# Kernel optimization log

Hardware: AMD Instinct MI355X
Metric: run time of the kernel (lower is better)

## Reference

```python
import jax, jax.numpy as jnp
import numpy as np
from jax import lax

M, T, WINDOW = 4096, 2048, 25
NEG_DIAG = -1e10  # matches alphas.fill_diagonal_(-1e10)


def setup_inputs() -> dict:
    key = jax.random.key(0)
    k_ys, k_a, k_r, k_b0, k_b1 = jax.random.split(key, 5)
    ys = jax.random.uniform(k_ys, (M, T), dtype=jnp.float32) * 10.0  # case counts
    alphas = 0.01 * jax.random.normal(k_a, (M, M), dtype=jnp.float32)
    repro = 1.0 + 0.01 * jax.random.normal(k_r, (M, WINDOW), dtype=jnp.float32)  # init ones
    b0 = 0.1 * jax.random.normal(k_b0, (M, 1), dtype=jnp.float32)
    b1 = 0.01 * jax.random.normal(k_b1, (M, 1), dtype=jnp.float32)
    t = jnp.arange(T, dtype=jnp.int32) + 1
    return {"ys": ys, "alphas": alphas, "repro": repro, "b0": b0, "b1": b1, "t": t}


def reference(ys, alphas, repro, b0, b1, t):
    m, _ = ys.shape
    window = repro.shape[1]
    offset = window - 1
    # metapopulation weights: sigmoid adjacency with diagonal forced to ~0
    diag = jnp.eye(m, dtype=bool)
    W = jax.nn.sigmoid(jnp.where(diag, jnp.asarray(NEG_DIAG, ys.dtype), alphas))
    # depthwise conv1d (cross-correlation), groups=M, VALID padding -> (M, T-window+1)
    Z = lax.conv_general_dilated(
        ys[None],                 # (1, M, T)
        repro[:, None, :],        # (M, 1, window)
        window_strides=(1,),
        padding='VALID',
        feature_group_count=m,
        dimension_numbers=('NCH', 'OIH', 'NCH'),
    )[0]                          # (M, T')
    ys_n = ys[:, offset:]         # (M, T')
    # beta_net: per-node softplus-linear in time -> (M, T), then narrow
    tt = t.astype(ys.dtype)
    beta = jax.nn.softplus(b0 + b1 * tt[None, :])[:, offset:]  # (M, T')
    return beta * (jax.nn.softplus(Z) + W @ ys_n)
```

## Files before the change

kernel.cpp:

```cpp
#include <hip/hip_runtime.h>
#include <stdint.h>

#define M_DIM 4096
#define T_DIM 2048
#define N_OUT 2024
#define N_PAD 2048
#define WIN   25
#define K_DIM 4096

typedef float f32x4 __attribute__((ext_vector_type(4)));

__device__ __forceinline__ unsigned short f2bf(float x) {
  unsigned u = __float_as_uint(x);
  u += 0x7FFF + ((u >> 16) & 1);
  return (unsigned short)(u >> 16);
}
__device__ __forceinline__ float bf2f(unsigned short h) {
  return __uint_as_float(((unsigned)h) << 16);
}

__device__ __forceinline__ void gl2lds16(const void* g, void* l) {
  __builtin_amdgcn_global_load_lds(
      (const __attribute__((address_space(1))) unsigned int*)g,
      (__attribute__((address_space(3))) unsigned int*)l, 16, 0, 0);
}

__device__ __forceinline__ int pk_fp8x4(float a, float b, float c, float d) {
  int w = __builtin_amdgcn_cvt_pk_fp8_f32(a, b, 0, false);
  w = __builtin_amdgcn_cvt_pk_fp8_f32(c, d, w, true);
  return w;
}

__global__ __launch_bounds__(256) void k_wcast(const float* __restrict__ alphas,
                                               unsigned char* __restrict__ W8) {
  size_t i8 = ((size_t)blockIdx.x * 256 + threadIdx.x) * 8;
  const float4 v0 = *(const float4*)(alphas + i8);
  const float4 v1 = *(const float4*)(alphas + i8 + 4);
  int row = (int)(i8 >> 12);
  int col = (int)(i8 & 4095);
  float a[8] = {v0.x, v0.y, v0.z, v0.w, v1.x, v1.y, v1.z, v1.w};
  float w[8];
#pragma unroll
  for (int j = 0; j < 8; ++j)
    w[j] = (row == col + j) ? 0.f : 1.f / (1.f + __expf(-a[j]));
  int p0 = pk_fp8x4(w[0], w[1], w[2], w[3]);
  int p1 = pk_fp8x4(w[4], w[5], w[6], w[7]);
  *(uint2*)(W8 + i8) = uint2{(unsigned)p0, (unsigned)p1};
}

__global__ __launch_bounds__(256) void k_conv(const float* __restrict__ ys,
                                              const float* __restrict__ repro,
                                              unsigned short* __restrict__ Sbf) {
  __shared__ float sy[256 + WIN - 1];
  __shared__ float sr[WIN];
  int m = blockIdx.y;
  int j0 = blockIdx.x * 256;
  int tid = threadIdx.x;
  sy[tid] = ys[(size_t)m * T_DIM + j0 + tid];
  if (tid < WIN - 1) {
    int jj = j0 + 256 + tid;
    sy[256 + tid] = (jj < T_DIM) ? ys[(size_t)m * T_DIM + jj] : 0.f;
  }
  if (tid < WIN) sr[tid] = repro[m * WIN + tid];
  __syncthreads();
  int j = j0 + tid;
  float z = 0.f;
#pragma unroll
  for (int k = 0; k < WIN; ++k) z += sy[tid + k] * sr[k];
  float sp = fmaxf(z, 0.f) + log1pf(__expf(-fabsf(z)));
  Sbf[(size_t)m * N_PAD + j] = (j < N_OUT) ? f2bf(sp) : (unsigned short)0;
}

__global__ __launch_bounds__(256) void k_transpose(const float* __restrict__ ys,
                                                   unsigned char* __restrict__ BT8) {
  __shared__ float t[64][65];
  int n0 = blockIdx.x * 64;
  int k0 = blockIdx.y * 64;
  int tx = threadIdx.x;
  int ty = threadIdx.y;
#pragma unroll
  for (int r = 0; r < 16; ++r) {
    int kk = k0 + ty + r * 4;
    int n = n0 + tx;
    t[ty + r * 4][tx] = (n < N_OUT) ? ys[(size_t)kk * T_DIM + n + (WIN - 1)] : 0.f;
  }
  __syncthreads();
  int tid = ty * 64 + tx;
  int nl = tid >> 2;
  int kc = (tid & 3) * 16;
  unsigned wds[4];
#pragma unroll
  for (int w = 0; w < 4; ++w)
    wds[w] = (unsigned)pk_fp8x4(t[kc + 4 * w][nl], t[kc + 4 * w + 1][nl],
                                t[kc + 4 * w + 2][nl], t[kc + 4 * w + 3][nl]);
  *(uint4*)(BT8 + (size_t)(n0 + nl) * K_DIM + k0 + kc) =
      uint4{wds[0], wds[1], wds[2], wds[3]};
}

__global__ __launch_bounds__(512, 4) void k_gemm(const unsigned char* __restrict__ W8,
                                                 const unsigned char* __restrict__ BT8,
                                                 const unsigned short* __restrict__ Sbf,
                                                 const float* __restrict__ b0,
                                                 const float* __restrict__ b1,
                                                 float* __restrict__ out) {
  __shared__ __align__(64) unsigned char lA[4][128 * 64];
  __shared__ __align__(64) unsigned char lB[4][128 * 64];
  const int tid  = threadIdx.x;
  const int wave = tid >> 6;
  const int lane = tid & 63;
  const int wm = wave >> 2;
  const int wn = wave & 3;
  const int m16  = lane & 15;
  const int quad = lane >> 4;

  const int fid  = blockIdx.y * gridDim.x + blockIdx.x;
  const int swz  = (fid & 7) * 64 + (fid >> 3);
  const int tileN = (swz & 15) * 128;
  const int tileM = (swz >> 4) * 128;

  const int key  = (m16 >> 1) & 3;
  const int sub  = (quad & 1) * 8;
  const int rowA = (wm * 64 + m16) * 64;
  const int rowB = (wn * 32 + m16) * 64;
  int hOf[2];
#pragma unroll
  for (int h = 0; h < 2; ++h)
    hOf[h] = (((2 * h + (quad >> 1)) ^ key) << 4) + sub;

  const int o = wave * 1024 + lane * 16;
  const int r = o >> 6;
  const int s = (o >> 4) & 3;
  const int q = s ^ ((r >> 1) & 3);
  const unsigned char* gA = W8  + (size_t)(tileM + r) * K_DIM + q * 16;
  const unsigned char* gB = BT8 + (size_t)(tileN + r) * K_DIM + q * 16;
  const int ldsOff = wave * 1024;

  f32x4 acc[4][2];
#pragma unroll
  for (int i = 0; i < 4; ++i)
#pragma unroll
    for (int j = 0; j < 2; ++j) acc[i][j] = f32x4{0.f, 0.f, 0.f, 0.f};

  auto stage = [&](int buf, int kt_) {
    const size_t kb_ = (size_t)kt_ * 64;
    gl2lds16(gA + kb_, &lA[buf][ldsOff]);
    gl2lds16(gB + kb_, &lB[buf][ldsOff]);
  };
  auto compute = [&](int buf) {
#pragma unroll
    for (int h = 0; h < 2; ++h) {
      long long aF[4], bF[2];
#pragma unroll
      for (int i = 0; i < 4; ++i)
        aF[i] = *(const long long*)&lA[buf][rowA + i * 1024 + hOf[h]];
#pragma unroll
      for (int j = 0; j < 2; ++j)
        bF[j] = *(const long long*)&lB[buf][rowB + j * 1024 + hOf[h]];
#pragma unroll
      for (int i = 0; i < 4; ++i)
#pragma unroll
        for (int j = 0; j < 2; ++j)
          acc[i][j] = __builtin_amdgcn_mfma_f32_16x16x32_fp8_fp8(
              aF[i], bF[j], acc[i][j], 0, 0, 0);
    }
  };

  stage(0, 0);
  stage(1, 1);
  stage(2, 2);

#pragma unroll 1
  for (int kt = 0; kt < K_DIM / 64; kt += 4) {
    stage(3, kt + 3);
    asm volatile("s_waitcnt vmcnt(6)" ::: "memory");
    __builtin_amdgcn_s_barrier();
    asm volatile("" ::: "memory");
    compute(0);
    __builtin_amdgcn_s_barrier();
    asm volatile("" ::: "memory");

    if (kt + 4 < K_DIM / 64) {
      stage(0, kt + 4);
      asm volatile("s_waitcnt vmcnt(6)" ::: "memory");
    } else {
      asm volatile("s_waitcnt vmcnt(4)" ::: "memory");
    }
    __builtin_amdgcn_s_barrier();
    asm volatile("" ::: "memory");
    compute(1);
    __builtin_amdgcn_s_barrier();
    asm volatile("" ::: "memory");

    if (kt + 5 < K_DIM / 64) {
      stage(1, kt + 5);
      asm volatile("s_waitcnt vmcnt(6)" ::: "memory");
    } else {
      asm volatile("s_waitcnt vmcnt(2)" ::: "memory");
    }
    __builtin_amdgcn_s_barrier();
    asm volatile("" ::: "memory");
    compute(2);
    __builtin_amdgcn_s_barrier();
    asm volatile("" ::: "memory");

    if (kt + 6 < K_DIM / 64) {
      stage(2, kt + 6);
      asm volatile("s_waitcnt vmcnt(6)" ::: "memory");
    } else {
      asm volatile("s_waitcnt vmcnt(0)" ::: "memory");
    }
    __builtin_amdgcn_s_barrier();
    asm volatile("" ::: "memory");
    compute(3);
    __builtin_amdgcn_s_barrier();
    asm volatile("" ::: "memory");
  }

#pragma unroll
  for (int j = 0; j < 2; ++j) {
    int gn = tileN + wn * 32 + j * 16 + m16;
    if (gn >= N_OUT) continue;
    float tval = (float)(gn + WIN);
#pragma unroll
    for (int i = 0; i < 4; ++i) {
#pragma unroll
      for (int r2 = 0; r2 < 4; ++r2) {
        int gm = tileM + wm * 64 + i * 16 + quad * 4 + r2;
        float x = b0[gm] + b1[gm] * tval;
        float beta = fmaxf(x, 0.f) + log1pf(__expf(-fabsf(x)));
        float sv = bf2f(Sbf[(size_t)gm * N_PAD + gn]);
        out[(size_t)gm * N_OUT + gn] = beta * (sv + acc[i][j][r2]);
      }
    }
  }
}

extern "C" void kernel_launch(void* const* d_in, const int* in_sizes, int n_in,
                              void* d_out, int out_size, void* d_ws, size_t ws_size,
                              hipStream_t stream) {
  const float* ys     = (const float*)d_in[0];
  const float* alphas = (const float*)d_in[1];
  const float* repro  = (const float*)d_in[2];
  const float* b0     = (const float*)d_in[3];
  const float* b1     = (const float*)d_in[4];
  float* out = (float*)d_out;

  char* ws = (char*)d_ws;
  unsigned char*  W8  = (unsigned char*)ws;
  unsigned char*  BT8 = (unsigned char*)(ws + (size_t)M_DIM * K_DIM);
  unsigned short* Sbf = (unsigned short*)(ws + (size_t)M_DIM * K_DIM
                                             + (size_t)N_PAD * K_DIM);

  k_wcast<<<(M_DIM * (size_t)K_DIM) / 8 / 256, 256, 0, stream>>>(alphas, W8);
  k_conv<<<dim3(T_DIM / 256, M_DIM), 256, 0, stream>>>(ys, repro, Sbf);
  k_transpose<<<dim3(N_PAD / 64, K_DIM / 64), dim3(64, 4), 0, stream>>>(ys, BT8);
  k_gemm<<<dim3(N_PAD / 128, M_DIM / 128), 512, 0, stream>>>(W8, BT8, Sbf, b0, b1, out);
}
```

Baseline: 252.7 us.

## Split-K GEMM with atomic accumulation and fuse prep kernels into one launch

Merges the weight cast, convolution, transpose and a new output-zeroing pass into a single block-dispatched prep kernel, which removes launch overhead. The GEMM now splits K into two halves across a third grid dimension, doubling the block count, and accumulates into the output with atomic adds. The LDS pipeline shrinks from four stages to two so more blocks fit per CU (launch bounds raised to 8). The cost is an extra zeroing pass over the output, atomic traffic on every output element, and a shallower prefetch pipeline.

```diff
diff --git a/kernel.cpp b/kernel.cpp
--- a/kernel.cpp
+++ b/kernel.cpp
@@ -7,6 +7,7 @@
 #define N_PAD 2048
 #define WIN   25
 #define K_DIM 4096
+#define K_HALF 2048
 
 typedef float f32x4 __attribute__((ext_vector_type(4)));
 
@@ -31,80 +32,96 @@
   return w;
 }
 
-__global__ __launch_bounds__(256) void k_wcast(const float* __restrict__ alphas,
-                                               unsigned char* __restrict__ W8) {
-  size_t i8 = ((size_t)blockIdx.x * 256 + threadIdx.x) * 8;
-  const float4 v0 = *(const float4*)(alphas + i8);
-  const float4 v1 = *(const float4*)(alphas + i8 + 4);
-  int row = (int)(i8 >> 12);
-  int col = (int)(i8 & 4095);
-  float a[8] = {v0.x, v0.y, v0.z, v0.w, v1.x, v1.y, v1.z, v1.w};
-  float w[8];
-#pragma unroll
-  for (int j = 0; j < 8; ++j)
-    w[j] = (row == col + j) ? 0.f : 1.f / (1.f + __expf(-a[j]));
-  int p0 = pk_fp8x4(w[0], w[1], w[2], w[3]);
-  int p1 = pk_fp8x4(w[4], w[5], w[6], w[7]);
-  *(uint2*)(W8 + i8) = uint2{(unsigned)p0, (unsigned)p1};
-}
-
-__global__ __launch_bounds__(256) void k_conv(const float* __restrict__ ys,
+#define NB_WCAST 8192
+#define NB_CONV  32768
+#define NB_TRANS 2048
+#define NB_ZERO  8096
+#define B_CONV   NB_WCAST
+#define B_TRANS  (B_CONV + NB_CONV)
+#define B_ZERO   (B_TRANS + NB_TRANS)
+#define NB_PREP  (B_ZERO + NB_ZERO)
+
+__global__ __launch_bounds__(256) void k_prep(const float* __restrict__ alphas,
+                                              const float* __restrict__ ys,
                                               const float* __restrict__ repro,
-                                              unsigned short* __restrict__ Sbf) {
-  __shared__ float sy[256 + WIN - 1];
-  __shared__ float sr[WIN];
-  int m = blockIdx.y;
-  int j0 = blockIdx.x * 256;
-  int tid = threadIdx.x;
-  sy[tid] = ys[(size_t)m * T_DIM + j0 + tid];
-  if (tid < WIN - 1) {
-    int jj = j0 + 256 + tid;
-    sy[256 + tid] = (jj < T_DIM) ? ys[(size_t)m * T_DIM + jj] : 0.f;
+                                              unsigned char* __restrict__ W8,
+                                              unsigned char* __restrict__ BT8,
+                                              unsigned short* __restrict__ Sbf,
+                                              float* __restrict__ out) {
+  __shared__ __align__(16) char smem[64 * 65 * 4];
+  const int bid = blockIdx.x;
+  const int tid = threadIdx.x;
+
+  if (bid < B_CONV) {
+    size_t i8 = ((size_t)bid * 256 + tid) * 8;
+    const float4 v0 = *(const float4*)(alphas + i8);
+    const float4 v1 = *(const float4*)(alphas + i8 + 4);
+    int row = (int)(i8 >> 12);
+    int col = (int)(i8 & 4095);
+    float a[8] = {v0.x, v0.y, v0.z, v0.w, v1.x, v1.y, v1.z, v1.w};
+    float w[8];
+#pragma unroll
+    for (int j = 0; j < 8; ++j)
+      w[j] = (row == col + j) ? 0.f : 1.f / (1.f + __expf(-a[j]));
+    int p0 = pk_fp8x4(w[0], w[1], w[2], w[3]);
+    int p1 = pk_fp8x4(w[4], w[5], w[6], w[7]);
+    *(uint2*)(W8 + i8) = uint2{(unsigned)p0, (unsigned)p1};
+  } else if (bid < B_TRANS) {
+    float* sy = (float*)smem;
+    float* sr = sy + 280;
+    int b  = bid - B_CONV;
+    int m  = b >> 3;
+    int j0 = (b & 7) * 256;
+    sy[tid] = ys[(size_t)m * T_DIM + j0 + tid];
+    if (tid < WIN - 1) {
+      int jj = j0 + 256 + tid;
+      sy[256 + tid] = (jj < T_DIM) ? ys[(size_t)m * T_DIM + jj] : 0.f;
+    }
+    if (tid < WIN) sr[tid] = repro[m * WIN + tid];
+    __syncthreads();
+    int j = j0 + tid;
+    float z = 0.f;
+#pragma unroll
+    for (int k = 0; k < WIN; ++k) z += sy[tid + k] * sr[k];
+    float sp = fmaxf(z, 0.f) + log1pf(__expf(-fabsf(z)));
+    Sbf[(size_t)m * N_PAD + j] = (j < N_OUT) ? f2bf(sp) : (unsigned short)0;
+  } else if (bid < B_ZERO) {
+    float (*t)[65] = (float (*)[65])smem;
+    int b  = bid - B_TRANS;
+    int n0 = (b & 31) * 64;
+    int k0 = (b >> 5) * 64;
+    int tx = tid & 63;
+    int ty = tid >> 6;
+#pragma unroll
+    for (int r = 0; r < 16; ++r) {
+      int kk = k0 + ty + r * 4;
+      int n = n0 + tx;
+      t[ty + r * 4][tx] = (n < N_OUT) ? ys[(size_t)kk * T_DIM + n + (WIN - 1)] : 0.f;
+    }
+    __syncthreads();
+    int nl = tid >> 2;
+    int kc = (tid & 3) * 16;
+    unsigned wds[4];
+#pragma unroll
+    for (int w = 0; w < 4; ++w)
+      wds[w] = (unsigned)pk_fp8x4(t[kc + 4 * w][nl], t[kc + 4 * w + 1][nl],
+                                  t[kc + 4 * w + 2][nl], t[kc + 4 * w + 3][nl]);
+    *(uint4*)(BT8 + (size_t)(n0 + nl) * K_DIM + k0 + kc) =
+        uint4{wds[0], wds[1], wds[2], wds[3]};
+  } else {
+    size_t idx = ((size_t)(bid - B_ZERO) * 256 + tid);
+    ((float4*)out)[idx] = float4{0.f, 0.f, 0.f, 0.f};
   }
-  if (tid < WIN) sr[tid] = repro[m * WIN + tid];
-  __syncthreads();
-  int j = j0 + tid;
-  float z = 0.f;
-#pragma unroll
-  for (int k = 0; k < WIN; ++k) z += sy[tid + k] * sr[k];
-  float sp = fmaxf(z, 0.f) + log1pf(__expf(-fabsf(z)));
-  Sbf[(size_t)m * N_PAD + j] = (j < N_OUT) ? f2bf(sp) : (unsigned short)0;
-}
-
-__global__ __launch_bounds__(256) void k_transpose(const float* __restrict__ ys,
-                                                   unsigned char* __restrict__ BT8) {
-  __shared__ float t[64][65];
-  int n0 = blockIdx.x * 64;
-  int k0 = blockIdx.y * 64;
-  int tx = threadIdx.x;
-  int ty = threadIdx.y;
-#pragma unroll
-  for (int r = 0; r < 16; ++r) {
-    int kk = k0 + ty + r * 4;
-    int n = n0 + tx;
-    t[ty + r * 4][tx] = (n < N_OUT) ? ys[(size_t)kk * T_DIM + n + (WIN - 1)] : 0.f;
-  }
-  __syncthreads();
-  int tid = ty * 64 + tx;
-  int nl = tid >> 2;
-  int kc = (tid & 3) * 16;
-  unsigned wds[4];
-#pragma unroll
-  for (int w = 0; w < 4; ++w)
-    wds[w] = (unsigned)pk_fp8x4(t[kc + 4 * w][nl], t[kc + 4 * w + 1][nl],
-                                t[kc + 4 * w + 2][nl], t[kc + 4 * w + 3][nl]);
-  *(uint4*)(BT8 + (size_t)(n0 + nl) * K_DIM + k0 + kc) =
-      uint4{wds[0], wds[1], wds[2], wds[3]};
-}
-
-__global__ __launch_bounds__(512, 4) void k_gemm(const unsigned char* __restrict__ W8,
+}
+
+__global__ __launch_bounds__(512, 8) void k_gemm(const unsigned char* __restrict__ W8,
                                                  const unsigned char* __restrict__ BT8,
                                                  const unsigned short* __restrict__ Sbf,
                                                  const float* __restrict__ b0,
                                                  const float* __restrict__ b1,
                                                  float* __restrict__ out) {
-  __shared__ __align__(64) unsigned char lA[4][128 * 64];
-  __shared__ __align__(64) unsigned char lB[4][128 * 64];
+  __shared__ __align__(64) unsigned char lA[2][128 * 64];
+  __shared__ __align__(64) unsigned char lB[2][128 * 64];
   const int tid  = threadIdx.x;
   const int wave = tid >> 6;
   const int lane = tid & 63;
@@ -113,10 +130,11 @@
   const int m16  = lane & 15;
   const int quad = lane >> 4;
 
-  const int fid  = blockIdx.y * gridDim.x + blockIdx.x;
-  const int swz  = (fid & 7) * 64 + (fid >> 3);
+  const int fid = (blockIdx.z * 32 + blockIdx.y) * 16 + blockIdx.x;
+  const int swz = (fid & 7) * 128 + (fid >> 3);
+  const int kh    = swz >> 9;
+  const int tileM = ((swz >> 4) & 31) * 128;
   const int tileN = (swz & 15) * 128;
-  const int tileM = (swz >> 4) * 128;
 
   const int key  = (m16 >> 1) & 3;
   const int sub  = (quad & 1) * 8;
@@ -131,8 +149,8 @@
   const int r = o >> 6;
   const int s = (o >> 4) & 3;
   const int q = s ^ ((r >> 1) & 3);
-  const unsigned char* gA = W8  + (size_t)(tileM + r) * K_DIM + q * 16;
-  const unsigned char* gB = BT8 + (size_t)(tileN + r) * K_DIM + q * 16;
+  const unsigned char* gA = W8  + (size_t)(tileM + r) * K_DIM + kh * K_HALF + q * 16;
+  const unsigned char* gB = BT8 + (size_t)(tileN + r) * K_DIM + kh * K_HALF + q * 16;
   const int ldsOff = wave * 1024;
 
   f32x4 acc[4][2];
@@ -166,52 +184,26 @@
   };
 
   stage(0, 0);
-  stage(1, 1);
-  stage(2, 2);
 
 #pragma unroll 1
-  for (int kt = 0; kt < K_DIM / 64; kt += 4) {
-    stage(3, kt + 3);
-    asm volatile("s_waitcnt vmcnt(6)" ::: "memory");
+  for (int kt = 0; kt < K_HALF / 64; kt += 2) {
+    stage(1, kt + 1);
+    asm volatile("s_waitcnt vmcnt(2)" ::: "memory");
     __builtin_amdgcn_s_barrier();
     asm volatile("" ::: "memory");
     compute(0);
     __builtin_amdgcn_s_barrier();
     asm volatile("" ::: "memory");
 
-    if (kt + 4 < K_DIM / 64) {
-      stage(0, kt + 4);
-      asm volatile("s_waitcnt vmcnt(6)" ::: "memory");
-    } else {
-      asm volatile("s_waitcnt vmcnt(4)" ::: "memory");
-    }
-    __builtin_amdgcn_s_barrier();
-    asm volatile("" ::: "memory");
-    compute(1);
-    __builtin_amdgcn_s_barrier();
-    asm volatile("" ::: "memory");
-
-    if (kt + 5 < K_DIM / 64) {
-      stage(1, kt + 5);
-      asm volatile("s_waitcnt vmcnt(6)" ::: "memory");
-    } else {
+    if (kt + 2 < K_HALF / 64) {
+      stage(0, kt + 2);
       asm volatile("s_waitcnt vmcnt(2)" ::: "memory");
-    }
-    __builtin_amdgcn_s_barrier();
-    asm volatile("" ::: "memory");
-    compute(2);
-    __builtin_amdgcn_s_barrier();
-    asm volatile("" ::: "memory");
-
-    if (kt + 6 < K_DIM / 64) {
-      stage(2, kt + 6);
-      asm volatile("s_waitcnt vmcnt(6)" ::: "memory");
     } else {
       asm volatile("s_waitcnt vmcnt(0)" ::: "memory");
     }
     __builtin_amdgcn_s_barrier();
     asm volatile("" ::: "memory");
-    compute(3);
+    compute(1);
     __builtin_amdgcn_s_barrier();
     asm volatile("" ::: "memory");
   }
@@ -228,8 +220,9 @@
         int gm = tileM + wm * 64 + i * 16 + quad * 4 + r2;
         float x = b0[gm] + b1[gm] * tval;
         float beta = fmaxf(x, 0.f) + log1pf(__expf(-fabsf(x)));
-        float sv = bf2f(Sbf[(size_t)gm * N_PAD + gn]);
-        out[(size_t)gm * N_OUT + gn] = beta * (sv + acc[i][j][r2]);
+        float sv = (kh == 0) ? bf2f(Sbf[(size_t)gm * N_PAD + gn]) : 0.f;
+        unsafeAtomicAdd(&out[(size_t)gm * N_OUT + gn],
+                        beta * (sv + acc[i][j][r2]));
       }
     }
   }
@@ -251,8 +244,7 @@
   unsigned short* Sbf = (unsigned short*)(ws + (size_t)M_DIM * K_DIM
                                              + (size_t)N_PAD * K_DIM);
 
-  k_wcast<<<(M_DIM * (size_t)K_DIM) / 8 / 256, 256, 0, stream>>>(alphas, W8);
-  k_conv<<<dim3(T_DIM / 256, M_DIM), 256, 0, stream>>>(ys, repro, Sbf);
-  k_transpose<<<dim3(N_PAD / 64, K_DIM / 64), dim3(64, 4), 0, stream>>>(ys, BT8);
-  k_gemm<<<dim3(N_PAD / 128, M_DIM / 128), 512, 0, stream>>>(W8, BT8, Sbf, b0, b1, out);
-}
+  k_prep<<<NB_PREP, 256, 0, stream>>>(alphas, ys, repro, W8, BT8, Sbf, out);
+  k_gemm<<<dim3(N_PAD / 128, M_DIM / 128, 2), 512, 0, stream>>>(W8, BT8, Sbf,
+                                                                b0, b1, out);
+}
```

Result: slower. 368.8 us (+46.0%).

## Merge prep kernels into one launch and widen GEMM block to 16 waves

Applied to the files above, without the earlier changes.

The W cast, conv/softplus and transpose kernels are folded into one launch that dispatches on block index, which removes two kernel launches and their serialization gaps. The FP8 GEMM block grows from 8 to 16 waves, each computing a 32x32 sub-tile. Waves 0-7 stage A and waves 8-15 stage B, so each wave issues one global-to-LDS load per stage and the vmcnt waits are halved to match. This raises the number of waves available to hide latency, but each MFMA now needs more LDS fragment reads and the tighter launch bounds may limit registers.

```diff
diff --git a/kernel.cpp b/kernel.cpp
--- a/kernel.cpp
+++ b/kernel.cpp
@@ -31,78 +31,88 @@
   return w;
 }
 
-__global__ __launch_bounds__(256) void k_wcast(const float* __restrict__ alphas,
-                                               unsigned char* __restrict__ W8) {
-  size_t i8 = ((size_t)blockIdx.x * 256 + threadIdx.x) * 8;
-  const float4 v0 = *(const float4*)(alphas + i8);
-  const float4 v1 = *(const float4*)(alphas + i8 + 4);
-  int row = (int)(i8 >> 12);
-  int col = (int)(i8 & 4095);
-  float a[8] = {v0.x, v0.y, v0.z, v0.w, v1.x, v1.y, v1.z, v1.w};
-  float w[8];
-#pragma unroll
-  for (int j = 0; j < 8; ++j)
-    w[j] = (row == col + j) ? 0.f : 1.f / (1.f + __expf(-a[j]));
-  int p0 = pk_fp8x4(w[0], w[1], w[2], w[3]);
-  int p1 = pk_fp8x4(w[4], w[5], w[6], w[7]);
-  *(uint2*)(W8 + i8) = uint2{(unsigned)p0, (unsigned)p1};
-}
-
-__global__ __launch_bounds__(256) void k_conv(const float* __restrict__ ys,
+#define NB_WCAST 8192
+#define NB_CONV  32768
+#define NB_TRANS 2048
+#define B_CONV   NB_WCAST
+#define B_TRANS  (B_CONV + NB_CONV)
+#define NB_PREP  (B_TRANS + NB_TRANS)
+
+__global__ __launch_bounds__(256) void k_prep(const float* __restrict__ alphas,
+                                              const float* __restrict__ ys,
                                               const float* __restrict__ repro,
+                                              unsigned char* __restrict__ W8,
+                                              unsigned char* __restrict__ BT8,
                                               unsigned short* __restrict__ Sbf) {
-  __shared__ float sy[256 + WIN - 1];
-  __shared__ float sr[WIN];
-  int m = blockIdx.y;
-  int j0 = blockIdx.x * 256;
-  int tid = threadIdx.x;
-  sy[tid] = ys[(size_t)m * T_DIM + j0 + tid];
-  if (tid < WIN - 1) {
-    int jj = j0 + 256 + tid;
-    sy[256 + tid] = (jj < T_DIM) ? ys[(size_t)m * T_DIM + jj] : 0.f;
+  __shared__ __align__(16) char smem[64 * 65 * 4];
+  const int bid = blockIdx.x;
+  const int tid = threadIdx.x;
+
+  if (bid < B_CONV) {
+    size_t i8 = ((size_t)bid * 256 + tid) * 8;
+    const float4 v0 = *(const float4*)(alphas + i8);
+    const float4 v1 = *(const float4*)(alphas + i8 + 4);
+    int row = (int)(i8 >> 12);
+    int col = (int)(i8 & 4095);
+    float a[8] = {v0.x, v0.y, v0.z, v0.w, v1.x, v1.y, v1.z, v1.w};
+    float w[8];
+#pragma unroll
+    for (int j = 0; j < 8; ++j)
+      w[j] = (row == col + j) ? 0.f : 1.f / (1.f + __expf(-a[j]));
+    int p0 = pk_fp8x4(w[0], w[1], w[2], w[3]);
+    int p1 = pk_fp8x4(w[4], w[5], w[6], w[7]);
+    *(uint2*)(W8 + i8) = uint2{(unsigned)p0, (unsigned)p1};
+  } else if (bid < B_TRANS) {
+    float* sy = (float*)smem;
+    float* sr = sy + 280;
+    int b  = bid - B_CONV;
+    int m  = b >> 3;
+    int j0 = (b & 7) * 256;
+    sy[tid] = ys[(size_t)m * T_DIM + j0 + tid];
+    if (tid < WIN - 1) {
+      int jj = j0 + 256 + tid;
+      sy[256 + tid] = (jj < T_DIM) ? ys[(size_t)m * T_DIM + jj] : 0.f;
+    }
+    if (tid < WIN) sr[tid] = repro[m * WIN + tid];
+    __syncthreads();
+    int j = j0 + tid;
+    float z = 0.f;
+#pragma unroll
+    for (int k = 0; k < WIN; ++k) z += sy[tid + k] * sr[k];
+    float sp = fmaxf(z, 0.f) + log1pf(__expf(-fabsf(z)));
+    Sbf[(size_t)m * N_PAD + j] = (j < N_OUT) ? f2bf(sp) : (unsigned short)0;
+  } else {
+    float (*t)[65] = (float (*)[65])smem;
+    int b  = bid - B_TRANS;
+    int n0 = (b & 31) * 64;
+    int k0 = (b >> 5) * 64;
+    int tx = tid & 63;
+    int ty = tid >> 6;
+#pragma unroll
+    for (int r = 0; r < 16; ++r) {
+      int kk = k0 + ty + r * 4;
+      int n = n0 + tx;
+      t[ty + r * 4][tx] = (n < N_OUT) ? ys[(size_t)kk * T_DIM + n + (WIN - 1)] : 0.f;
+    }
+    __syncthreads();
+    int nl = tid >> 2;
+    int kc = (tid & 3) * 16;
+    unsigned wds[4];
+#pragma unroll
+    for (int w = 0; w < 4; ++w)
+      wds[w] = (unsigned)pk_fp8x4(t[kc + 4 * w][nl], t[kc + 4 * w + 1][nl],
+                                  t[kc + 4 * w + 2][nl], t[kc + 4 * w + 3][nl]);
+    *(uint4*)(BT8 + (size_t)(n0 + nl) * K_DIM + k0 + kc) =
+        uint4{wds[0], wds[1], wds[2], wds[3]};
   }
-  if (tid < WIN) sr[tid] = repro[m * WIN + tid];
-  __syncthreads();
-  int j = j0 + tid;
-  float z = 0.f;
-#pragma unroll
-  for (int k = 0; k < WIN; ++k) z += sy[tid + k] * sr[k];
-  float sp = fmaxf(z, 0.f) + log1pf(__expf(-fabsf(z)));
-  Sbf[(size_t)m * N_PAD + j] = (j < N_OUT) ? f2bf(sp) : (unsigned short)0;
-}
-
-__global__ __launch_bounds__(256) void k_transpose(const float* __restrict__ ys,
-                                                   unsigned char* __restrict__ BT8) {
-  __shared__ float t[64][65];
-  int n0 = blockIdx.x * 64;
-  int k0 = blockIdx.y * 64;
-  int tx = threadIdx.x;
-  int ty = threadIdx.y;
-#pragma unroll
-  for (int r = 0; r < 16; ++r) {
-    int kk = k0 + ty + r * 4;
-    int n = n0 + tx;
-    t[ty + r * 4][tx] = (n < N_OUT) ? ys[(size_t)kk * T_DIM + n + (WIN - 1)] : 0.f;
-  }
-  __syncthreads();
-  int tid = ty * 64 + tx;
-  int nl = tid >> 2;
-  int kc = (tid & 3) * 16;
-  unsigned wds[4];
-#pragma unroll
-  for (int w = 0; w < 4; ++w)
-    wds[w] = (unsigned)pk_fp8x4(t[kc + 4 * w][nl], t[kc + 4 * w + 1][nl],
-                                t[kc + 4 * w + 2][nl], t[kc + 4 * w + 3][nl]);
-  *(uint4*)(BT8 + (size_t)(n0 + nl) * K_DIM + k0 + kc) =
-      uint4{wds[0], wds[1], wds[2], wds[3]};
-}
-
-__global__ __launch_bounds__(512, 4) void k_gemm(const unsigned char* __restrict__ W8,
-                                                 const unsigned char* __restrict__ BT8,
-                                                 const unsigned short* __restrict__ Sbf,
-                                                 const float* __restrict__ b0,
-                                                 const float* __restrict__ b1,
-                                                 float* __restrict__ out) {
+}
+
+__global__ __launch_bounds__(1024, 8) void k_gemm(const unsigned char* __restrict__ W8,
+                                                  const unsigned char* __restrict__ BT8,
+                                                  const unsigned short* __restrict__ Sbf,
+                                                  const float* __restrict__ b0,
+                                                  const float* __restrict__ b1,
+                                                  float* __restrict__ out) {
   __shared__ __align__(64) unsigned char lA[4][128 * 64];
   __shared__ __align__(64) unsigned char lB[4][128 * 64];
   const int tid  = threadIdx.x;
@@ -120,44 +130,46 @@
 
   const int key  = (m16 >> 1) & 3;
   const int sub  = (quad & 1) * 8;
-  const int rowA = (wm * 64 + m16) * 64;
+  const int rowA = (wm * 32 + m16) * 64;
   const int rowB = (wn * 32 + m16) * 64;
   int hOf[2];
 #pragma unroll
   for (int h = 0; h < 2; ++h)
     hOf[h] = (((2 * h + (quad >> 1)) ^ key) << 4) + sub;
 
-  const int o = wave * 1024 + lane * 16;
-  const int r = o >> 6;
-  const int s = (o >> 4) & 3;
-  const int q = s ^ ((r >> 1) & 3);
-  const unsigned char* gA = W8  + (size_t)(tileM + r) * K_DIM + q * 16;
-  const unsigned char* gB = BT8 + (size_t)(tileN + r) * K_DIM + q * 16;
-  const int ldsOff = wave * 1024;
-
-  f32x4 acc[4][2];
-#pragma unroll
-  for (int i = 0; i < 4; ++i)
+  const int sw = wave & 7;
+  const int o  = sw * 1024 + lane * 16;
+  const int r  = o >> 6;
+  const int s  = (o >> 4) & 3;
+  const int q  = s ^ ((r >> 1) & 3);
+  const bool isA = (wave < 8);
+  const unsigned char* gSrc =
+      (isA ? W8 + (size_t)(tileM + r) * K_DIM
+           : BT8 + (size_t)(tileN + r) * K_DIM) + q * 16;
+  const int ldsOff = sw * 1024;
+
+  f32x4 acc[2][2];
+#pragma unroll
+  for (int i = 0; i < 2; ++i)
 #pragma unroll
     for (int j = 0; j < 2; ++j) acc[i][j] = f32x4{0.f, 0.f, 0.f, 0.f};
 
   auto stage = [&](int buf, int kt_) {
     const size_t kb_ = (size_t)kt_ * 64;
-    gl2lds16(gA + kb_, &lA[buf][ldsOff]);
-    gl2lds16(gB + kb_, &lB[buf][ldsOff]);
+    gl2lds16(gSrc + kb_, (isA ? &lA[buf][ldsOff] : &lB[buf][ldsOff]));
   };
   auto compute = [&](int buf) {
 #pragma unroll
     for (int h = 0; h < 2; ++h) {
-      long long aF[4], bF[2];
-#pragma unroll
-      for (int i = 0; i < 4; ++i)
+      long long aF[2], bF[2];
+#pragma unroll
+      for (int i = 0; i < 2; ++i)
         aF[i] = *(const long long*)&lA[buf][rowA + i * 1024 + hOf[h]];
 #pragma unroll
       for (int j = 0; j < 2; ++j)
         bF[j] = *(const long long*)&lB[buf][rowB + j * 1024 + hOf[h]];
 #pragma unroll
-      for (int i = 0; i < 4; ++i)
+      for (int i = 0; i < 2; ++i)
 #pragma unroll
         for (int j = 0; j < 2; ++j)
           acc[i][j] = __builtin_amdgcn_mfma_f32_16x16x32_fp8_fp8(
@@ -172,7 +184,7 @@
 #pragma unroll 1
   for (int kt = 0; kt < K_DIM / 64; kt += 4) {
     stage(3, kt + 3);
-    asm volatile("s_waitcnt vmcnt(6)" ::: "memory");
+    asm volatile("s_waitcnt vmcnt(3)" ::: "memory");
     __builtin_amdgcn_s_barrier();
     asm volatile("" ::: "memory");
     compute(0);
@@ -181,9 +193,9 @@
 
     if (kt + 4 < K_DIM / 64) {
       stage(0, kt + 4);
-      asm volatile("s_waitcnt vmcnt(6)" ::: "memory");
+      asm volatile("s_waitcnt vmcnt(3)" ::: "memory");
     } else {
-      asm volatile("s_waitcnt vmcnt(4)" ::: "memory");
+      asm volatile("s_waitcnt vmcnt(2)" ::: "memory");
     }
     __builtin_amdgcn_s_barrier();
     asm volatile("" ::: "memory");
@@ -193,9 +205,9 @@
 
     if (kt + 5 < K_DIM / 64) {
       stage(1, kt + 5);
-      asm volatile("s_waitcnt vmcnt(6)" ::: "memory");
+      asm volatile("s_waitcnt vmcnt(3)" ::: "memory");
     } else {
-      asm volatile("s_waitcnt vmcnt(2)" ::: "memory");
+      asm volatile("s_waitcnt vmcnt(1)" ::: "memory");
     }
     __builtin_amdgcn_s_barrier();
     asm volatile("" ::: "memory");
@@ -205,7 +217,7 @@
 
     if (kt + 6 < K_DIM / 64) {
       stage(2, kt + 6);
-      asm volatile("s_waitcnt vmcnt(6)" ::: "memory");
+      asm volatile("s_waitcnt vmcnt(3)" ::: "memory");
     } else {
       asm volatile("s_waitcnt vmcnt(0)" ::: "memory");
     }
@@ -222,10 +234,10 @@
     if (gn >= N_OUT) continue;
     float tval = (float)(gn + WIN);
 #pragma unroll
-    for (int i = 0; i < 4; ++i) {
+    for (int i = 0; i < 2; ++i) {
 #pragma unroll
       for (int r2 = 0; r2 < 4; ++r2) {
-        int gm = tileM + wm * 64 + i * 16 + quad * 4 + r2;
+        int gm = tileM + wm * 32 + i * 16 + quad * 4 + r2;
         float x = b0[gm] + b1[gm] * tval;
         float beta = fmaxf(x, 0.f) + log1pf(__expf(-fabsf(x)));
         float sv = bf2f(Sbf[(size_t)gm * N_PAD + gn]);
@@ -251,8 +263,7 @@
   unsigned short* Sbf = (unsigned short*)(ws + (size_t)M_DIM * K_DIM
                                              + (size_t)N_PAD * K_DIM);
 
-  k_wcast<<<(M_DIM * (size_t)K_DIM) / 8 / 256, 256, 0, stream>>>(alphas, W8);
-  k_conv<<<dim3(T_DIM / 256, M_DIM), 256, 0, stream>>>(ys, repro, Sbf);
-  k_transpose<<<dim3(N_PAD / 64, K_DIM / 64), dim3(64, 4), 0, stream>>>(ys, BT8);
-  k_gemm<<<dim3(N_PAD / 128, M_DIM / 128), 512, 0, stream>>>(W8, BT8, Sbf, b0, b1, out);
-}
+  k_prep<<<NB_PREP, 256, 0, stream>>>(alphas, ys, repro, W8, BT8, Sbf);
+  k_gemm<<<dim3(N_PAD / 128, M_DIM / 128), 1024, 0, stream>>>(W8, BT8, Sbf,
+                                                              b0, b1, out);
+}
```

Measured after the change: 258.6 us. 2.3% more time.

## Fuse prep kernels and GEMM into one cooperative persistent kernel with grid sync

Applied to the files above, without the earlier changes.

Merges the weight cast, conv+softplus, and transpose kernels into a single prep phase run by 512 blocks of 512 threads. It then runs the FP8 GEMM in the same launch, separated by a cooperative grid-wide barrier. The aim is to remove three launch gaps and tail effects, and to restructure the conv so each wave handles a row with register windows. The price is a grid sync, and a fallback to two kernels if the cooperative launch fails. Prep work is also redistributed, which may lower its parallelism.

```diff
diff --git a/kernel.cpp b/kernel.cpp
--- a/kernel.cpp
+++ b/kernel.cpp
@@ -1,5 +1,8 @@
 #include <hip/hip_runtime.h>
+#include <hip/hip_cooperative_groups.h>
 #include <stdint.h>
+
+namespace cg = cooperative_groups;
 
 #define M_DIM 4096
 #define T_DIM 2048
@@ -31,81 +34,110 @@
   return w;
 }
 
-__global__ __launch_bounds__(256) void k_wcast(const float* __restrict__ alphas,
-                                               unsigned char* __restrict__ W8) {
-  size_t i8 = ((size_t)blockIdx.x * 256 + threadIdx.x) * 8;
-  const float4 v0 = *(const float4*)(alphas + i8);
-  const float4 v1 = *(const float4*)(alphas + i8 + 4);
-  int row = (int)(i8 >> 12);
-  int col = (int)(i8 & 4095);
-  float a[8] = {v0.x, v0.y, v0.z, v0.w, v1.x, v1.y, v1.z, v1.w};
-  float w[8];
-#pragma unroll
-  for (int j = 0; j < 8; ++j)
-    w[j] = (row == col + j) ? 0.f : 1.f / (1.f + __expf(-a[j]));
-  int p0 = pk_fp8x4(w[0], w[1], w[2], w[3]);
-  int p1 = pk_fp8x4(w[4], w[5], w[6], w[7]);
-  *(uint2*)(W8 + i8) = uint2{(unsigned)p0, (unsigned)p1};
-}
-
-__global__ __launch_bounds__(256) void k_conv(const float* __restrict__ ys,
-                                              const float* __restrict__ repro,
-                                              unsigned short* __restrict__ Sbf) {
-  __shared__ float sy[256 + WIN - 1];
-  __shared__ float sr[WIN];
-  int m = blockIdx.y;
-  int j0 = blockIdx.x * 256;
-  int tid = threadIdx.x;
-  sy[tid] = ys[(size_t)m * T_DIM + j0 + tid];
-  if (tid < WIN - 1) {
-    int jj = j0 + 256 + tid;
-    sy[256 + tid] = (jj < T_DIM) ? ys[(size_t)m * T_DIM + jj] : 0.f;
-  }
-  if (tid < WIN) sr[tid] = repro[m * WIN + tid];
-  __syncthreads();
-  int j = j0 + tid;
-  float z = 0.f;
-#pragma unroll
-  for (int k = 0; k < WIN; ++k) z += sy[tid + k] * sr[k];
-  float sp = fmaxf(z, 0.f) + log1pf(__expf(-fabsf(z)));
-  Sbf[(size_t)m * N_PAD + j] = (j < N_OUT) ? f2bf(sp) : (unsigned short)0;
-}
-
-__global__ __launch_bounds__(256) void k_transpose(const float* __restrict__ ys,
-                                                   unsigned char* __restrict__ BT8) {
-  __shared__ float t[64][65];
-  int n0 = blockIdx.x * 64;
-  int k0 = blockIdx.y * 64;
-  int tx = threadIdx.x;
-  int ty = threadIdx.y;
-#pragma unroll
-  for (int r = 0; r < 16; ++r) {
-    int kk = k0 + ty + r * 4;
-    int n = n0 + tx;
-    t[ty + r * 4][tx] = (n < N_OUT) ? ys[(size_t)kk * T_DIM + n + (WIN - 1)] : 0.f;
-  }
-  __syncthreads();
-  int tid = ty * 64 + tx;
-  int nl = tid >> 2;
-  int kc = (tid & 3) * 16;
-  unsigned wds[4];
-#pragma unroll
-  for (int w = 0; w < 4; ++w)
-    wds[w] = (unsigned)pk_fp8x4(t[kc + 4 * w][nl], t[kc + 4 * w + 1][nl],
-                                t[kc + 4 * w + 2][nl], t[kc + 4 * w + 3][nl]);
-  *(uint4*)(BT8 + (size_t)(n0 + nl) * K_DIM + k0 + kc) =
-      uint4{wds[0], wds[1], wds[2], wds[3]};
-}
-
-__global__ __launch_bounds__(512, 4) void k_gemm(const unsigned char* __restrict__ W8,
-                                                 const unsigned char* __restrict__ BT8,
-                                                 const unsigned short* __restrict__ Sbf,
-                                                 const float* __restrict__ b0,
-                                                 const float* __restrict__ b1,
-                                                 float* __restrict__ out) {
-  __shared__ __align__(64) unsigned char lA[4][128 * 64];
-  __shared__ __align__(64) unsigned char lB[4][128 * 64];
-  const int tid  = threadIdx.x;
+__device__ __forceinline__ void prep_body(int bid, int tid,
+                                          const float* __restrict__ alphas,
+                                          const float* __restrict__ ys,
+                                          const float* __restrict__ repro,
+                                          unsigned char* __restrict__ W8,
+                                          unsigned char* __restrict__ BT8,
+                                          unsigned short* __restrict__ Sbf,
+                                          char* SMEM) {
+  {
+    int idx = bid * 512 + tid;
+#pragma unroll
+    for (int itr = 0; itr < 8; ++itr) {
+      size_t i8 = ((size_t)idx + (size_t)itr * 262144) * 8;
+      const float4 v0 = *(const float4*)(alphas + i8);
+      const float4 v1 = *(const float4*)(alphas + i8 + 4);
+      int row = (int)(i8 >> 12);
+      int col = (int)(i8 & 4095);
+      float a[8] = {v0.x, v0.y, v0.z, v0.w, v1.x, v1.y, v1.z, v1.w};
+      float w[8];
+#pragma unroll
+      for (int j = 0; j < 8; ++j)
+        w[j] = (row == col + j) ? 0.f : 1.f / (1.f + __expf(-a[j]));
+      int p0 = pk_fp8x4(w[0], w[1], w[2], w[3]);
+      int p1 = pk_fp8x4(w[4], w[5], w[6], w[7]);
+      *(uint2*)(W8 + i8) = uint2{(unsigned)p0, (unsigned)p1};
+    }
+  }
+
+  {
+    int m = bid * 8 + (tid >> 6);
+    int lane = tid & 63;
+    float r[WIN];
+#pragma unroll
+    for (int k = 0; k < WIN; ++k) r[k] = repro[m * WIN + k];
+#pragma unroll
+    for (int p = 0; p < 2; ++p) {
+      int c0 = lane * 32 + p * 16;
+      float y[16 + WIN - 1];
+#pragma unroll
+      for (int ch = 0; ch < 10; ++ch) {
+        int c = c0 + ch * 4;
+        float4 v = (c + 3 < T_DIM) ? *(const float4*)(ys + (size_t)m * T_DIM + c)
+                                   : float4{0.f, 0.f, 0.f, 0.f};
+        y[ch * 4 + 0] = v.x; y[ch * 4 + 1] = v.y;
+        y[ch * 4 + 2] = v.z; y[ch * 4 + 3] = v.w;
+      }
+      unsigned short ob[16];
+#pragma unroll
+      for (int j = 0; j < 16; ++j) {
+        float z = 0.f;
+#pragma unroll
+        for (int k = 0; k < WIN; ++k) z += y[j + k] * r[k];
+        float sp = fmaxf(z, 0.f) + log1pf(__expf(-fabsf(z)));
+        int gj = c0 + j;
+        ob[j] = (gj < N_OUT) ? f2bf(sp) : (unsigned short)0;
+      }
+      unsigned short* dst = Sbf + (size_t)m * N_PAD + c0;
+      *(uint4*)dst = ((const uint4*)ob)[0];
+      *(uint4*)(dst + 8) = ((const uint4*)ob)[1];
+    }
+  }
+
+  {
+    int half = tid >> 8;
+    int st   = tid & 255;
+    float (*t)[65] = (float (*)[65])(SMEM + half * 16640);
+    int tx = st & 63;
+    int ty = st >> 6;
+#pragma unroll 1
+    for (int it = 0; it < 2; ++it) {
+      int b  = bid * 4 + it * 2 + half;
+      int n0 = (b & 31) * 64;
+      int k0 = (b >> 5) * 64;
+#pragma unroll
+      for (int rr = 0; rr < 16; ++rr) {
+        int kk = k0 + ty + rr * 4;
+        int n = n0 + tx;
+        t[ty + rr * 4][tx] = (n < N_OUT) ? ys[(size_t)kk * T_DIM + n + (WIN - 1)] : 0.f;
+      }
+      __syncthreads();
+      int nl = st >> 2;
+      int kc = (st & 3) * 16;
+      unsigned wds[4];
+#pragma unroll
+      for (int w = 0; w < 4; ++w)
+        wds[w] = (unsigned)pk_fp8x4(t[kc + 4 * w][nl], t[kc + 4 * w + 1][nl],
+                                    t[kc + 4 * w + 2][nl], t[kc + 4 * w + 3][nl]);
+      *(uint4*)(BT8 + (size_t)(n0 + nl) * K_DIM + k0 + kc) =
+          uint4{wds[0], wds[1], wds[2], wds[3]};
+      __syncthreads();
+    }
+  }
+}
+
+__device__ __forceinline__ void gemm_body(int bid, int tid,
+                                          const unsigned char* __restrict__ W8,
+                                          const unsigned char* __restrict__ BT8,
+                                          const unsigned short* __restrict__ Sbf,
+                                          const float* __restrict__ b0,
+                                          const float* __restrict__ b1,
+                                          float* __restrict__ out,
+                                          char* SMEM) {
+  unsigned char* lA = (unsigned char*)SMEM;
+  unsigned char* lB = (unsigned char*)SMEM + 32768;
   const int wave = tid >> 6;
   const int lane = tid & 63;
   const int wm = wave >> 2;
@@ -113,8 +145,7 @@
   const int m16  = lane & 15;
   const int quad = lane >> 4;
 
-  const int fid  = blockIdx.y * gridDim.x + blockIdx.x;
-  const int swz  = (fid & 7) * 64 + (fid >> 3);
+  const int swz  = (bid & 7) * 64 + (bid >> 3);
   const int tileN = (swz & 15) * 128;
   const int tileM = (swz >> 4) * 128;
 
@@ -143,8 +174,8 @@
 
   auto stage = [&](int buf, int kt_) {
     const size_t kb_ = (size_t)kt_ * 64;
-    gl2lds16(gA + kb_, &lA[buf][ldsOff]);
-    gl2lds16(gB + kb_, &lB[buf][ldsOff]);
+    gl2lds16(gA + kb_, lA + buf * 8192 + ldsOff);
+    gl2lds16(gB + kb_, lB + buf * 8192 + ldsOff);
   };
   auto compute = [&](int buf) {
 #pragma unroll
@@ -152,10 +183,10 @@
       long long aF[4], bF[2];
 #pragma unroll
       for (int i = 0; i < 4; ++i)
-        aF[i] = *(const long long*)&lA[buf][rowA + i * 1024 + hOf[h]];
+        aF[i] = *(const long long*)(lA + buf * 8192 + rowA + i * 1024 + hOf[h]);
 #pragma unroll
       for (int j = 0; j < 2; ++j)
-        bF[j] = *(const long long*)&lB[buf][rowB + j * 1024 + hOf[h]];
+        bF[j] = *(const long long*)(lB + buf * 8192 + rowB + j * 1024 + hOf[h]);
 #pragma unroll
       for (int i = 0; i < 4; ++i)
 #pragma unroll
@@ -233,6 +264,43 @@
       }
     }
   }
+}
+
+__global__ __launch_bounds__(512, 4) void k_fused(const float* __restrict__ ys,
+                                                  const float* __restrict__ alphas,
+                                                  const float* __restrict__ repro,
+                                                  const float* __restrict__ b0,
+                                                  const float* __restrict__ b1,
+                                                  unsigned char* __restrict__ W8,
+                                                  unsigned char* __restrict__ BT8,
+                                                  unsigned short* __restrict__ Sbf,
+                                                  float* __restrict__ out) {
+  __shared__ __align__(64) char SMEM[65536];
+  const int bid = blockIdx.x;
+  const int tid = threadIdx.x;
+  prep_body(bid, tid, alphas, ys, repro, W8, BT8, Sbf, SMEM);
+  __threadfence();
+  cg::this_grid().sync();
+  gemm_body(bid, tid, W8, BT8, Sbf, b0, b1, out, SMEM);
+}
+
+__global__ __launch_bounds__(512, 4) void k_prep2(const float* __restrict__ ys,
+                                                  const float* __restrict__ alphas,
+                                                  const float* __restrict__ repro,
+                                                  unsigned char* __restrict__ W8,
+                                                  unsigned char* __restrict__ BT8,
+                                                  unsigned short* __restrict__ Sbf) {
+  __shared__ __align__(64) char SMEM[65536];
+  prep_body(blockIdx.x, threadIdx.x, alphas, ys, repro, W8, BT8, Sbf, SMEM);
+}
+__global__ __launch_bounds__(512, 4) void k_gemm2(const unsigned char* __restrict__ W8,
+                                                  const unsigned char* __restrict__ BT8,
+                                                  const unsigned short* __restrict__ Sbf,
+                                                  const float* __restrict__ b0,
+                                                  const float* __restrict__ b1,
+                                                  float* __restrict__ out) {
+  __shared__ __align__(64) char SMEM[65536];
+  gemm_body(blockIdx.x, threadIdx.x, W8, BT8, Sbf, b0, b1, out, SMEM);
 }
 
 extern "C" void kernel_launch(void* const* d_in, const int* in_sizes, int n_in,
@@ -251,8 +319,12 @@
   unsigned short* Sbf = (unsigned short*)(ws + (size_t)M_DIM * K_DIM
                                              + (size_t)N_PAD * K_DIM);
 
-  k_wcast<<<(M_DIM * (size_t)K_DIM) / 8 / 256, 256, 0, stream>>>(alphas, W8);
-  k_conv<<<dim3(T_DIM / 256, M_DIM), 256, 0, stream>>>(ys, repro, Sbf);
-  k_transpose<<<dim3(N_PAD / 64, K_DIM / 64), dim3(64, 4), 0, stream>>>(ys, BT8);
-  k_gemm<<<dim3(N_PAD / 128, M_DIM / 128), 512, 0, stream>>>(W8, BT8, Sbf, b0, b1, out);
-}
+  void* args[] = {(void*)&ys, (void*)&alphas, (void*)&repro, (void*)&b0,
+                  (void*)&b1, (void*)&W8, (void*)&BT8, (void*)&Sbf, (void*)&out};
+  hipError_t e = hipLaunchCooperativeKernel((const void*)k_fused, dim3(512),
+                                            dim3(512), args, 0, stream);
+  if (e != hipSuccess) {
+    k_prep2<<<512, 512, 0, stream>>>(ys, alphas, repro, W8, BT8, Sbf);
+    k_gemm2<<<512, 512, 0, stream>>>(W8, BT8, Sbf, b0, b1, out);
+  }
+}
```

After: 437.0 us. 1.73x slower.
